# Kernel tuning notes

Hardware: AMD Instinct MI355X
Metric: run time of the kernel (lower is better)

## Reference

```python
import jax, jax.numpy as jnp
import numpy as np

B, S, D, H = 2, 2048, 1024, 16
HD = D // H  # head_dim = 64


def setup_inputs() -> dict:
    key = jax.random.key(0)
    k1, k2, k3 = jax.random.split(key, 3)
    x = jax.random.normal(k1, (B, S, D), dtype=jnp.float32)
    mask = jnp.zeros((B, S, S), dtype=jnp.float32)  # additive mask
    # Dense(3*D) params (glorot-ish scale) and Dense(D) output projection
    Wqkv = jax.random.normal(k2, (D, 3 * D), dtype=jnp.float32) * (1.0 / np.sqrt(D))
    bqkv = jnp.zeros((3 * D,), dtype=jnp.float32)
    Wo = jax.random.normal(k3, (D, D), dtype=jnp.float32) * (1.0 / np.sqrt(D))
    bo = jnp.zeros((D,), dtype=jnp.float32)
    return {"x": x, "mask": mask, "Wqkv": Wqkv, "bqkv": bqkv, "Wo": Wo, "bo": bo}


def reference(x, mask, Wqkv, bqkv, Wo, bo):
    b, s, d = x.shape
    qkv = x @ Wqkv + bqkv                              # [B,S,3D]
    qkv = qkv.reshape(b, s, H, 3 * HD).transpose(0, 2, 1, 3)  # [B,H,S,3*HD]
    q, k, v = jnp.split(qkv, 3, axis=-1)               # each [B,H,S,HD]
    scale = 1.0 / jnp.sqrt(jnp.float32(HD))
    scores = jnp.einsum('bhqd,bhkd->bhqk', q, k) * scale  # [B,H,S,S]
    scores = scores + mask[:, None, :, :]
    attn = jax.nn.softmax(scores, axis=-1)
    values = jnp.einsum('bhqk,bhkd->bhqd', attn, v)    # [B,H,S,HD]
    # Faithful to original: reshape WITHOUT transposing heads back
    values = values.reshape(b, s, H * HD)              # [B,S,D]
    return values @ Wo + bo
```

## Files before the change

### kernel.cpp

```cpp
#include <hip/hip_runtime.h>
#include <hip/hip_bf16.h>

#define B_ 2
#define S_ 2048
#define D_ 1024
#define H_ 16
#define HD_ 64

typedef __attribute__((ext_vector_type(8))) short short8;
typedef __attribute__((ext_vector_type(4))) float f32x4;
typedef __attribute__((ext_vector_type(4))) unsigned short us4;

static __device__ __forceinline__ ushort f2bf(float x) {
  __hip_bfloat16 h = __float2bfloat16(x);
  return *reinterpret_cast<ushort*>(&h);
}

static __device__ __forceinline__ void gld_lds16(void* lds, const void* g) {
  __builtin_amdgcn_global_load_lds(
      (__attribute__((address_space(1))) void*)(g),
      (__attribute__((address_space(3))) void*)(lds), 16, 0, 0);
}


__global__ __launch_bounds__(256) void cvt_bf16_vec(const float4* __restrict__ in,
                                                    ushort* __restrict__ out, int n4) {
  int i = blockIdx.x * blockDim.x + threadIdx.x;
  if (i < n4) {
    float4 v = in[i];
    ushort4 o;
    o.x = f2bf(v.x); o.y = f2bf(v.y); o.z = f2bf(v.z); o.w = f2bf(v.w);
    *reinterpret_cast<ushort4*>(out + (size_t)i * 4) = o;
  }
}

__global__ __launch_bounds__(256) void transpose_cvt(const float* __restrict__ in,
                                                     ushort* __restrict__ out,
                                                     int K, int N) {
  __shared__ float tile[32][33];
  const int bn = blockIdx.x * 32, bk = blockIdx.y * 32;
  const int tx = threadIdx.x, ty = threadIdx.y;
  #pragma unroll
  for (int i = ty; i < 32; i += 8)
    tile[i][tx] = in[(size_t)(bk + i) * N + bn + tx];
  __syncthreads();
  #pragma unroll
  for (int i = ty; i < 32; i += 8)
    out[(size_t)(bn + i) * K + bk + tx] = f2bf(tile[tx][i]);
}

template <bool OUT_BF16>
__global__ __launch_bounds__(256) void gemm_bt(const ushort* __restrict__ A,
                                               const ushort* __restrict__ Bt,
                                               const float* __restrict__ bias,
                                               ushort* __restrict__ Cb,
                                               float* __restrict__ Cf,
                                               int M, int N, int K) {
  __shared__ __align__(16) ushort As[128 * 32];
  __shared__ __align__(16) ushort Bs[128 * 32];
  const int tid = threadIdx.x;
  const int lane = tid & 63, wid = tid >> 6;
  const int wr = wid >> 1, wc = wid & 1;
  const int row0 = blockIdx.x * 128, col0 = blockIdx.y * 128;
  const int l15 = lane & 15, lhi = lane >> 4;

  f32x4 acc[4][4];
  #pragma unroll
  for (int i = 0; i < 4; ++i)
    #pragma unroll
    for (int j = 0; j < 4; ++j)
      acc[i][j] = f32x4{0.f, 0.f, 0.f, 0.f};

  const int sr = tid >> 2;
  const int scol = (tid & 3) * 8;

  for (int k0 = 0; k0 < K; k0 += 32) {
    gld_lds16(&As[(size_t)tid * 8],        &A[(size_t)(row0 + sr) * K + k0 + scol]);
    gld_lds16(&As[2048 + (size_t)tid * 8], &A[(size_t)(row0 + 64 + sr) * K + k0 + scol]);
    gld_lds16(&Bs[(size_t)tid * 8],        &Bt[(size_t)(col0 + sr) * K + k0 + scol]);
    gld_lds16(&Bs[2048 + (size_t)tid * 8], &Bt[(size_t)(col0 + 64 + sr) * K + k0 + scol]);
    __syncthreads();

    short8 af[4], bfr[4];
    #pragma unroll
    for (int mt = 0; mt < 4; ++mt)
      af[mt] = *(const short8*)&As[(wr * 64 + mt * 16 + l15) * 32 + lhi * 8];
    #pragma unroll
    for (int nt = 0; nt < 4; ++nt)
      bfr[nt] = *(const short8*)&Bs[(wc * 64 + nt * 16 + l15) * 32 + lhi * 8];
    #pragma unroll
    for (int mt = 0; mt < 4; ++mt)
      #pragma unroll
      for (int nt = 0; nt < 4; ++nt)
        acc[mt][nt] = __builtin_amdgcn_mfma_f32_16x16x32_bf16(af[mt], bfr[nt], acc[mt][nt], 0, 0, 0);
    __syncthreads();
  }

  const int orow = row0 + wr * 64;
  const int ocol = col0 + wc * 64 + l15;
  #pragma unroll
  for (int mt = 0; mt < 4; ++mt) {
    #pragma unroll
    for (int nt = 0; nt < 4; ++nt) {
      const int gc = ocol + nt * 16;
      const float bv = bias[gc];
      #pragma unroll
      for (int r = 0; r < 4; ++r) {
        const int gr = orow + mt * 16 + lhi * 4 + r;
        const float v = acc[mt][nt][r] + bv;
        if (OUT_BF16) Cb[(size_t)gr * N + gc] = f2bf(v);
        else          Cf[(size_t)gr * N + gc] = v;
      }
    }
  }
}

__global__ __launch_bounds__(256, 4) void flash_attn(const ushort* __restrict__ qkv,
                                                     const float* __restrict__ mask,
                                                     ushort* __restrict__ values) {
  __shared__ __align__(16) ushort Ks[2][64 * 64];
  __shared__ __align__(16) ushort Vt[2][64 * 64];

  const int tid = threadIdx.x;
  const int lane = tid & 63, wid = tid >> 6;
  const int l15 = lane & 15, lhi = lane >> 4;
  const int qt = blockIdx.x, bh = blockIdx.y, b = bh >> 4, h = bh & 15;
  const size_t base = (size_t)b * S_ * 3072 + (size_t)h * 192;
  const int q = qt * 64 + wid * 16 + l15;

  short8 qf0, qf1;
  {
    const ushort* qrow = qkv + base + (size_t)q * 3072 + lhi * 8;
    qf0 = *(const short8*)qrow;
    qf1 = *(const short8*)(qrow + 32);
  }

  const int srow = tid >> 3, sch = tid & 7;
  const int scs = sch ^ ((srow & 3) | ((srow & 8) >> 1));
  const int kg = tid & 15, d0 = (tid >> 4) * 4;
  const int hkr = (l15 & 3) | (((l15 >> 2) & 1) << 2);
  const int klbase = ((l15 >> 2) << 3) | (l15 & 3);

  float m_run = -3.0e38f, l_run = 0.f;
  f32x4 o[4];
  #pragma unroll
  for (int dt = 0; dt < 4; ++dt) o[dt] = f32x4{0.f, 0.f, 0.f, 0.f};

  const float* mrow = mask + ((size_t)b * S_ + q) * S_;
  const int NT = S_ / 64;
  int cur = 0;
  us4 vr[4];

  {
    const ushort* kg0 = qkv + base + (size_t)srow * 3072 + 64;
    gld_lds16(&Ks[0][tid * 8],        kg0 + scs * 8);
    gld_lds16(&Ks[0][2048 + tid * 8], kg0 + (size_t)32 * 3072 + scs * 8);
    #pragma unroll
    for (int kk = 0; kk < 4; ++kk)
      vr[kk] = *(const us4*)(qkv + base + (size_t)(kg * 4 + kk) * 3072 + 128 + d0);
    #pragma unroll
    for (int dd = 0; dd < 3 + 1; ++dd) {
      const int d = d0 + dd;
      us4 w;
      w[0] = vr[0][dd]; w[1] = vr[1][dd]; w[2] = vr[2][dd]; w[3] = vr[3][dd];
      *(us4*)&Vt[0][d * 64 + (((kg >> 1) ^ (d & 7)) * 8) + (kg & 1) * 4] = w;
    }
    __syncthreads();
  }

  for (int kt = 0; kt < NT; ++kt) {
    const int nxt = cur ^ 1;
    const bool pre = (kt + 1 < NT);

    if (pre) {
      const ushort* kgn = qkv + base + (size_t)(kt + 1) * 64 * 3072 + (size_t)srow * 3072 + 64;
      gld_lds16(&Ks[nxt][tid * 8],        kgn + scs * 8);
      gld_lds16(&Ks[nxt][2048 + tid * 8], kgn + (size_t)32 * 3072 + scs * 8);
      #pragma unroll
      for (int kk = 0; kk < 4; ++kk)
        vr[kk] = *(const us4*)(qkv + base + (size_t)(kt + 1) * 64 * 3072 +
                               (size_t)(kg * 4 + kk) * 3072 + 128 + d0);
    }

    f32x4 mk[4];
    {
      const float* mp = mrow + kt * 64 + lhi * 8;
      mk[0] = *(const f32x4*)(mp);
      mk[1] = *(const f32x4*)(mp + 4);
      mk[2] = *(const f32x4*)(mp + 32);
      mk[3] = *(const f32x4*)(mp + 36);
    }

    f32x4 sc[4];
    __builtin_amdgcn_s_setprio(1);
    #pragma unroll
    for (int m = 0; m < 4; ++m) {
      const int kl = (m >> 1) * 32 + (m & 1) * 4 + klbase;
      const int c1 = (lhi ^ hkr) & 7;
      const ushort* kp = &Ks[cur][kl * 64];
      short8 kf0 = *(const short8*)&kp[c1 * 8];
      short8 kf1 = *(const short8*)&kp[(c1 ^ 4) * 8];
      f32x4 s = f32x4{0.f, 0.f, 0.f, 0.f};
      s = __builtin_amdgcn_mfma_f32_16x16x32_bf16(kf0, qf0, s, 0, 0, 0);
      s = __builtin_amdgcn_mfma_f32_16x16x32_bf16(kf1, qf1, s, 0, 0, 0);
      sc[m] = s;
    }
    __builtin_amdgcn_s_setprio(0);

    #pragma unroll
    for (int m = 0; m < 4; ++m)
      #pragma unroll
      for (int r = 0; r < 4; ++r)
        sc[m][r] = sc[m][r] * 0.125f + mk[m][r];

    float mx = sc[0][0];
    #pragma unroll
    for (int m = 0; m < 4; ++m)
      #pragma unroll
      for (int r = 0; r < 4; ++r) mx = fmaxf(mx, sc[m][r]);
    mx = fmaxf(mx, __shfl_xor(mx, 16));
    mx = fmaxf(mx, __shfl_xor(mx, 32));
    const float mnew = fmaxf(m_run, mx);
    const float alpha = __expf(m_run - mnew);
    m_run = mnew;
    float ps = 0.f;
    #pragma unroll
    for (int m = 0; m < 4; ++m)
      #pragma unroll
      for (int r = 0; r < 4; ++r) {
        const float p = __expf(sc[m][r] - mnew);
        sc[m][r] = p;
        ps += p;
      }
    ps += __shfl_xor(ps, 16);
    ps += __shfl_xor(ps, 32);
    l_run = l_run * alpha + ps;
    #pragma unroll
    for (int dt = 0; dt < 4; ++dt)
      #pragma unroll
      for (int r = 0; r < 4; ++r) o[dt][r] *= alpha;

    short8 pf[2];
    #pragma unroll
    for (int c = 0; c < 2; ++c)
      #pragma unroll
      for (int j = 0; j < 8; ++j)
        pf[c][j] = (short)f2bf(sc[c * 2 + (j >> 2)][j & 3]);

    __builtin_amdgcn_s_setprio(1);
    #pragma unroll
    for (int dt = 0; dt < 4; ++dt) {
      const int d = dt * 16 + l15;
      const ushort* vp = &Vt[cur][d * 64];
      #pragma unroll
      for (int c = 0; c < 2; ++c) {
        short8 vf = *(const short8*)&vp[(((c * 4 + lhi) ^ (d & 7)) & 7) * 8];
        o[dt] = __builtin_amdgcn_mfma_f32_16x16x32_bf16(vf, pf[c], o[dt], 0, 0, 0);
      }
    }
    __builtin_amdgcn_s_setprio(0);

    if (pre) {
      #pragma unroll
      for (int dd = 0; dd < 4; ++dd) {
        const int d = d0 + dd;
        us4 w;
        w[0] = vr[0][dd]; w[1] = vr[1][dd]; w[2] = vr[2][dd]; w[3] = vr[3][dd];
        *(us4*)&Vt[nxt][d * 64 + (((kg >> 1) ^ (d & 7)) * 8) + (kg & 1) * 4] = w;
      }
    }
    __syncthreads();
    cur = nxt;
  }

  const float inv = 1.0f / l_run;
  ushort* vout = values + ((size_t)bh * S_ + q) * 64 + lhi * 4;
  #pragma unroll
  for (int dt = 0; dt < 4; ++dt) {
    us4 w;
    #pragma unroll
    for (int r = 0; r < 4; ++r) w[r] = f2bf(o[dt][r] * inv);
    *(us4*)(vout + dt * 16) = w;
  }
}


extern "C" void kernel_launch(void* const* d_in, const int* in_sizes, int n_in,
                              void* d_out, int out_size, void* d_ws, size_t ws_size,
                              hipStream_t stream) {
  const float* x    = (const float*)d_in[0];
  const float* mask = (const float*)d_in[1];
  const float* Wqkv = (const float*)d_in[2];
  const float* bqkv = (const float*)d_in[3];
  const float* Wo   = (const float*)d_in[4];
  const float* bo   = (const float*)d_in[5];
  float* out = (float*)d_out;

  char* ws = (char*)d_ws;
  ushort* xbf    = (ushort*)(ws + 0);
  ushort* vals   = (ushort*)(ws + 0);
  ushort* wqkvT  = (ushort*)(ws + 8388608);
  ushort* woT    = (ushort*)(ws + 14680064);
  ushort* qkv    = (ushort*)(ws + 16777216);

  cvt_bf16_vec<<<4096, 256, 0, stream>>>((const float4*)x, xbf, (B_ * S_ * D_) / 4);
  transpose_cvt<<<dim3(3 * D_ / 32, D_ / 32), dim3(32, 8), 0, stream>>>(Wqkv, wqkvT, D_, 3 * D_);
  transpose_cvt<<<dim3(D_ / 32, D_ / 32), dim3(32, 8), 0, stream>>>(Wo, woT, D_, D_);
  gemm_bt<true><<<dim3((B_ * S_) / 128, (3 * D_) / 128), 256, 0, stream>>>(
      xbf, wqkvT, bqkv, qkv, nullptr, B_ * S_, 3 * D_, D_);
  flash_attn<<<dim3(S_ / 64, B_ * H_), 256, 0, stream>>>(qkv, mask, vals);
  gemm_bt<false><<<dim3((B_ * S_) / 128, D_ / 128), 256, 0, stream>>>(
      vals, woT, bo, nullptr, out, B_ * S_, D_, D_);
}
```

Before: 215.6 us.

## Switch flash attention to 32x32x16 MFMA with 128-query tiles

```diff
diff --git a/kernel.cpp b/kernel.cpp
--- a/kernel.cpp
+++ b/kernel.cpp
@@ -9,6 +9,7 @@
 
 typedef __attribute__((ext_vector_type(8))) short short8;
 typedef __attribute__((ext_vector_type(4))) float f32x4;
+typedef __attribute__((ext_vector_type(16))) float f32x16;
 typedef __attribute__((ext_vector_type(4))) unsigned short us4;
 
 static __device__ __forceinline__ ushort f2bf(float x) {
@@ -115,7 +116,7 @@
   }
 }
 
-__global__ __launch_bounds__(256, 4) void flash_attn(const ushort* __restrict__ qkv,
+__global__ __launch_bounds__(256, 2) void flash_attn(const ushort* __restrict__ qkv,
                                                      const float* __restrict__ mask,
                                                      ushort* __restrict__ values) {
   __shared__ __align__(16) ushort Ks[2][64 * 64];
@@ -123,47 +124,56 @@
 
   const int tid = threadIdx.x;
   const int lane = tid & 63, wid = tid >> 6;
-  const int l15 = lane & 15, lhi = lane >> 4;
+  const int l31 = lane & 31, lhalf = lane >> 5;
   const int qt = blockIdx.x, bh = blockIdx.y, b = bh >> 4, h = bh & 15;
   const size_t base = (size_t)b * S_ * 3072 + (size_t)h * 192;
-  const int q = qt * 64 + wid * 16 + l15;
-
-  short8 qf0, qf1;
+  const int q = qt * 128 + wid * 32 + l31;
+
+  short8 qf[4];
   {
-    const ushort* qrow = qkv + base + (size_t)q * 3072 + lhi * 8;
-    qf0 = *(const short8*)qrow;
-    qf1 = *(const short8*)(qrow + 32);
+    const ushort* qrow = qkv + base + (size_t)q * 3072 + lhalf * 8;
+    qf[0] = *(const short8*)(qrow);
+    qf[1] = *(const short8*)(qrow + 16);
+    qf[2] = *(const short8*)(qrow + 32);
+    qf[3] = *(const short8*)(qrow + 48);
   }
 
   const int srow = tid >> 3, sch = tid & 7;
-  const int scs = sch ^ ((srow & 3) | ((srow & 8) >> 1));
+  const int hsr = (srow ^ (srow >> 3)) & 7;
+  const int scs = sch ^ hsr;
   const int kg = tid & 15, d0 = (tid >> 4) * 4;
-  const int hkr = (l15 & 3) | (((l15 >> 2) & 1) << 2);
-  const int klbase = ((l15 >> 2) << 3) | (l15 & 3);
+  const int skg = (kg & 12) | ((kg & 1) << 1) | ((kg >> 1) & 1);
 
   float m_run = -3.0e38f, l_run = 0.f;
-  f32x4 o[4];
-  #pragma unroll
-  for (int dt = 0; dt < 4; ++dt) o[dt] = f32x4{0.f, 0.f, 0.f, 0.f};
+  f32x16 o[2];
+  #pragma unroll
+  for (int dg = 0; dg < 2; ++dg)
+    #pragma unroll
+    for (int i = 0; i < 16; ++i) o[dg][i] = 0.f;
 
   const float* mrow = mask + ((size_t)b * S_ + q) * S_;
+  f32x4 mk[8], mkn[8];
   const int NT = S_ / 64;
   int cur = 0;
   us4 vr[4];
 
   {
-    const ushort* kg0 = qkv + base + (size_t)srow * 3072 + 64;
-    gld_lds16(&Ks[0][tid * 8],        kg0 + scs * 8);
-    gld_lds16(&Ks[0][2048 + tid * 8], kg0 + (size_t)32 * 3072 + scs * 8);
+    const ushort* kgp = qkv + base + (size_t)srow * 3072 + 64;
+    gld_lds16(&Ks[0][tid * 8],        kgp + scs * 8);
+    gld_lds16(&Ks[0][2048 + tid * 8], kgp + (size_t)32 * 3072 + (scs ^ 4) * 8);
     #pragma unroll
     for (int kk = 0; kk < 4; ++kk)
       vr[kk] = *(const us4*)(qkv + base + (size_t)(kg * 4 + kk) * 3072 + 128 + d0);
     #pragma unroll
-    for (int dd = 0; dd < 3 + 1; ++dd) {
+    for (int i = 0; i < 8; ++i)
+      mk[i] = *(const f32x4*)(mrow + (i >> 2) * 32 + (i & 3) * 8 + lhalf * 4);
+    #pragma unroll
+    for (int dd = 0; dd < 4; ++dd) {
       const int d = d0 + dd;
+      const int hd = (d ^ (d >> 3)) & 7;
       us4 w;
       w[0] = vr[0][dd]; w[1] = vr[1][dd]; w[2] = vr[2][dd]; w[3] = vr[3][dd];
-      *(us4*)&Vt[0][d * 64 + (((kg >> 1) ^ (d & 7)) * 8) + (kg & 1) * 4] = w;
+      *(us4*)&Vt[0][d * 64 + (((skg >> 1) ^ hd) & 7) * 8 + (skg & 1) * 4] = w;
     }
     __syncthreads();
   }
@@ -173,89 +183,86 @@
     const bool pre = (kt + 1 < NT);
 
     if (pre) {
-      const ushort* kgn = qkv + base + (size_t)(kt + 1) * 64 * 3072 + (size_t)srow * 3072 + 64;
-      gld_lds16(&Ks[nxt][tid * 8],        kgn + scs * 8);
-      gld_lds16(&Ks[nxt][2048 + tid * 8], kgn + (size_t)32 * 3072 + scs * 8);
+      const size_t nb = base + (size_t)(kt + 1) * 64 * 3072;
+      const ushort* kgp = qkv + nb + (size_t)srow * 3072 + 64;
+      gld_lds16(&Ks[nxt][tid * 8],        kgp + scs * 8);
+      gld_lds16(&Ks[nxt][2048 + tid * 8], kgp + (size_t)32 * 3072 + (scs ^ 4) * 8);
       #pragma unroll
       for (int kk = 0; kk < 4; ++kk)
-        vr[kk] = *(const us4*)(qkv + base + (size_t)(kt + 1) * 64 * 3072 +
-                               (size_t)(kg * 4 + kk) * 3072 + 128 + d0);
-    }
-
-    f32x4 mk[4];
-    {
-      const float* mp = mrow + kt * 64 + lhi * 8;
-      mk[0] = *(const f32x4*)(mp);
-      mk[1] = *(const f32x4*)(mp + 4);
-      mk[2] = *(const f32x4*)(mp + 32);
-      mk[3] = *(const f32x4*)(mp + 36);
-    }
-
-    f32x4 sc[4];
+        vr[kk] = *(const us4*)(qkv + nb + (size_t)(kg * 4 + kk) * 3072 + 128 + d0);
+      const float* mn = mrow + (size_t)(kt + 1) * 64;
+      #pragma unroll
+      for (int i = 0; i < 8; ++i)
+        mkn[i] = *(const f32x4*)(mn + (i >> 2) * 32 + (i & 3) * 8 + lhalf * 4);
+    }
+
+    f32x16 sc[2];
     __builtin_amdgcn_s_setprio(1);
     #pragma unroll
-    for (int m = 0; m < 4; ++m) {
-      const int kl = (m >> 1) * 32 + (m & 1) * 4 + klbase;
-      const int c1 = (lhi ^ hkr) & 7;
-      const ushort* kp = &Ks[cur][kl * 64];
-      short8 kf0 = *(const short8*)&kp[c1 * 8];
-      short8 kf1 = *(const short8*)&kp[(c1 ^ 4) * 8];
-      f32x4 s = f32x4{0.f, 0.f, 0.f, 0.f};
-      s = __builtin_amdgcn_mfma_f32_16x16x32_bf16(kf0, qf0, s, 0, 0, 0);
-      s = __builtin_amdgcn_mfma_f32_16x16x32_bf16(kf1, qf1, s, 0, 0, 0);
-      sc[m] = s;
+    for (int g = 0; g < 2; ++g) {
+      const int row = g * 32 + l31;
+      const int hk = (row ^ (row >> 3)) & 7;
+      const ushort* kp = &Ks[cur][row * 64];
+      f32x16 s;
+      #pragma unroll
+      for (int i = 0; i < 16; ++i) s[i] = 0.f;
+      #pragma unroll
+      for (int kd = 0; kd < 4; ++kd) {
+        short8 kf = *(const short8*)&kp[(((kd * 2 + lhalf) ^ hk) & 7) * 8];
+        s = __builtin_amdgcn_mfma_f32_32x32x16_bf16(kf, qf[kd], s, 0, 0, 0);
+      }
+      sc[g] = s;
     }
     __builtin_amdgcn_s_setprio(0);
 
     #pragma unroll
-    for (int m = 0; m < 4; ++m)
-      #pragma unroll
-      for (int r = 0; r < 4; ++r)
-        sc[m][r] = sc[m][r] * 0.125f + mk[m][r];
+    for (int g = 0; g < 2; ++g)
+      #pragma unroll
+      for (int r = 0; r < 16; ++r)
+        sc[g][r] = sc[g][r] * 0.125f + mk[g * 4 + (r >> 2)][r & 3];
 
     float mx = sc[0][0];
     #pragma unroll
-    for (int m = 0; m < 4; ++m)
-      #pragma unroll
-      for (int r = 0; r < 4; ++r) mx = fmaxf(mx, sc[m][r]);
-    mx = fmaxf(mx, __shfl_xor(mx, 16));
+    for (int g = 0; g < 2; ++g)
+      #pragma unroll
+      for (int r = 0; r < 16; ++r) mx = fmaxf(mx, sc[g][r]);
     mx = fmaxf(mx, __shfl_xor(mx, 32));
     const float mnew = fmaxf(m_run, mx);
     const float alpha = __expf(m_run - mnew);
     m_run = mnew;
     float ps = 0.f;
     #pragma unroll
-    for (int m = 0; m < 4; ++m)
-      #pragma unroll
-      for (int r = 0; r < 4; ++r) {
-        const float p = __expf(sc[m][r] - mnew);
-        sc[m][r] = p;
+    for (int g = 0; g < 2; ++g)
+      #pragma unroll
+      for (int r = 0; r < 16; ++r) {
+        const float p = __expf(sc[g][r] - mnew);
+        sc[g][r] = p;
         ps += p;
       }
-    ps += __shfl_xor(ps, 16);
     ps += __shfl_xor(ps, 32);
     l_run = l_run * alpha + ps;
     #pragma unroll
-    for (int dt = 0; dt < 4; ++dt)
-      #pragma unroll
-      for (int r = 0; r < 4; ++r) o[dt][r] *= alpha;
-
-    short8 pf[2];
-    #pragma unroll
-    for (int c = 0; c < 2; ++c)
+    for (int dg = 0; dg < 2; ++dg)
+      #pragma unroll
+      for (int i = 0; i < 16; ++i) o[dg][i] *= alpha;
+
+    short8 pf[4];
+    #pragma unroll
+    for (int ks = 0; ks < 4; ++ks)
       #pragma unroll
       for (int j = 0; j < 8; ++j)
-        pf[c][j] = (short)f2bf(sc[c * 2 + (j >> 2)][j & 3]);
+        pf[ks][j] = (short)f2bf(sc[ks >> 1][8 * (ks & 1) + j]);
 
     __builtin_amdgcn_s_setprio(1);
     #pragma unroll
-    for (int dt = 0; dt < 4; ++dt) {
-      const int d = dt * 16 + l15;
+    for (int dg = 0; dg < 2; ++dg) {
+      const int d = dg * 32 + l31;
+      const int hv = (d ^ (d >> 3)) & 7;
       const ushort* vp = &Vt[cur][d * 64];
       #pragma unroll
-      for (int c = 0; c < 2; ++c) {
-        short8 vf = *(const short8*)&vp[(((c * 4 + lhi) ^ (d & 7)) & 7) * 8];
-        o[dt] = __builtin_amdgcn_mfma_f32_16x16x32_bf16(vf, pf[c], o[dt], 0, 0, 0);
+      for (int ks = 0; ks < 4; ++ks) {
+        short8 vf = *(const short8*)&vp[(((ks * 2 + lhalf) ^ hv) & 7) * 8];
+        o[dg] = __builtin_amdgcn_mfma_f32_32x32x16_bf16(vf, pf[ks], o[dg], 0, 0, 0);
       }
     }
     __builtin_amdgcn_s_setprio(0);
@@ -264,24 +271,29 @@
       #pragma unroll
       for (int dd = 0; dd < 4; ++dd) {
         const int d = d0 + dd;
+        const int hd = (d ^ (d >> 3)) & 7;
         us4 w;
         w[0] = vr[0][dd]; w[1] = vr[1][dd]; w[2] = vr[2][dd]; w[3] = vr[3][dd];
-        *(us4*)&Vt[nxt][d * 64 + (((kg >> 1) ^ (d & 7)) * 8) + (kg & 1) * 4] = w;
-      }
+        *(us4*)&Vt[nxt][d * 64 + (((skg >> 1) ^ hd) & 7) * 8 + (skg & 1) * 4] = w;
+      }
+      #pragma unroll
+      for (int i = 0; i < 8; ++i) mk[i] = mkn[i];
     }
     __syncthreads();
     cur = nxt;
   }
 
   const float inv = 1.0f / l_run;
-  ushort* vout = values + ((size_t)bh * S_ + q) * 64 + lhi * 4;
-  #pragma unroll
-  for (int dt = 0; dt < 4; ++dt) {
-    us4 w;
-    #pragma unroll
-    for (int r = 0; r < 4; ++r) w[r] = f2bf(o[dt][r] * inv);
-    *(us4*)(vout + dt * 16) = w;
-  }
+  ushort* vout = values + ((size_t)bh * S_ + q) * 64;
+  #pragma unroll
+  for (int dg = 0; dg < 2; ++dg)
+    #pragma unroll
+    for (int quad = 0; quad < 4; ++quad) {
+      us4 w;
+      #pragma unroll
+      for (int r = 0; r < 4; ++r) w[r] = f2bf(o[dg][quad * 4 + r] * inv);
+      *(us4*)(vout + dg * 32 + quad * 8 + lhalf * 4) = w;
+    }
 }
 
 
@@ -308,7 +320,7 @@
   transpose_cvt<<<dim3(D_ / 32, D_ / 32), dim3(32, 8), 0, stream>>>(Wo, woT, D_, D_);
   gemm_bt<true><<<dim3((B_ * S_) / 128, (3 * D_) / 128), 256, 0, stream>>>(
       xbf, wqkvT, bqkv, qkv, nullptr, B_ * S_, 3 * D_, D_);
-  flash_attn<<<dim3(S_ / 64, B_ * H_), 256, 0, stream>>>(qkv, mask, vals);
+  flash_attn<<<dim3(S_ / 128, B_ * H_), 256, 0, stream>>>(qkv, mask, vals);
   gemm_bt<false><<<dim3((B_ * S_) / 128, D_ / 128), 256, 0, stream>>>(
       vals, woT, bo, nullptr, out, B_ * S_, D_, D_);
 }
```

Result: faster. 180.4 us (-16.3%).
